# Kernel tuning notes

Measured on AMD Instinct MI355X. Metric: run time of the kernel, lower is better.

The kernel has to match this reference:

```python
import jax, jax.numpy as jnp
import numpy as np

TEMPERATURE = 0.07
NEG = -1e30  # safe stand-in for -inf (keeps grads NaN-free)


def setup_inputs() -> dict:
    key = jax.random.key(0)
    k1, k2 = jax.random.split(key)
    semantic_state = jax.random.normal(k1, (8, 1024, 64), dtype=jnp.float32)
    token_ids = jax.random.randint(k2, (8, 1024), 0, 1000)
    return {"semantic_state": semantic_state, "token_ids": token_ids}


def reference(semantic_state, token_ids):
    # semantic_state: [B, T, D], token_ids: [B, T]
    B, T, D = semantic_state.shape
    N = B * T
    x = semantic_state.reshape(N, D)
    tok = token_ids.reshape(N)

    # L2 normalize (F.normalize, eps=1e-12)
    nrm = jnp.sqrt(jnp.sum(x * x, axis=1, keepdims=True))
    z = x / jnp.maximum(nrm, 1e-12)

    # full cosine-similarity matrix [N, N]
    S = z @ z.T

    # pairs: same token id, excluding self (the per-group similarity structure)
    same = tok[:, None] == tok[None, :]
    eye = jnp.eye(N, dtype=bool)
    mask = same & ~eye

    # per-anchor contrastive term: -logsumexp_{j != i, tok_j == tok_i}(-S_ij / T)
    logits = jnp.where(mask, -S / TEMPERATURE, NEG)
    lse = jax.nn.logsumexp(logits, axis=1)

    valid = mask.any(axis=1)  # anchors whose token repeats (count >= 2)
    per_anchor = jnp.where(valid, -lse, 0.0)

    num_pairs = jnp.sum(mask)  # == sum over groups of N_g*(N_g-1)
    loss = jnp.where(
        num_pairs > 0,
        jnp.sum(per_anchor) / jnp.maximum(num_pairs, 1).astype(S.dtype),
        jnp.array(0.0, dtype=S.dtype),
    )
    return loss
```

## Files before the change

### kernel.cpp

```cpp
#include <hip/hip_runtime.h>
#include <math.h>

#define TEMP 0.07f
#define NTOK 1024
#define CAP 64

__global__ __launch_bounds__(256) void prep_kernel(const float* __restrict__ x,
        const int* __restrict__ tok, float* __restrict__ invn,
        int* __restrict__ cursor, int* __restrict__ bucket, int n) {
    const int lane = threadIdx.x & 63;
    const int w = blockIdx.x * 4 + (threadIdx.x >> 6);
    const int sub = lane & 15, grp = lane >> 4;
    const int row = w * 4 + grp;
    if (row >= n) return;
    float4 v = *(const float4*)&x[row * 64 + sub * 4];
    float s = v.x * v.x + v.y * v.y + v.z * v.z + v.w * v.w;
    s += __shfl_xor(s, 1, 64);
    s += __shfl_xor(s, 2, 64);
    s += __shfl_xor(s, 4, 64);
    s += __shfl_xor(s, 8, 64);
    if (sub == 0) {
        invn[row] = 1.0f / fmaxf(sqrtf(s), 1e-12f);
        int g = tok[row];
        int slot = atomicAdd(&cursor[g], 1);
        if (slot < CAP) bucket[g * CAP + slot] = row;
    }
}

__global__ __launch_bounds__(256) void lse_kernel(const float* __restrict__ x,
        const int* __restrict__ tok, const float* __restrict__ invn,
        const int* __restrict__ cursor, const int* __restrict__ bucket,
        float* __restrict__ per_anchor, int n) {
    const int lane = threadIdx.x & 63;
    const int i = blockIdx.x * 4 + (threadIdx.x >> 6);
    if (i >= n) return;
    const int g = tok[i];
    const int cnt = min(cursor[g], CAP);
    if (cnt < 2) {
        if (lane == 0) per_anchor[i] = 0.0f;
        return;
    }
    const int sub = lane & 15, grp = lane >> 4;
    float4 zi = *(const float4*)&x[i * 64 + sub * 4];
    float sc = invn[i] * (1.0f / TEMP);
    zi.x *= sc; zi.y *= sc; zi.z *= sc; zi.w *= sc;
    const int* bk = &bucket[g * CAP];
    float S = 0.0f;
    for (int m0 = 0; m0 < cnt; m0 += 4) {
        int mm = m0 + grp;
        bool act = (mm < cnt);
        int j = act ? bk[mm] : 0;
        act = act && (j != i);
        float4 zj = *(const float4*)&x[j * 64 + sub * 4];
        float iv = invn[j];
        float d = zi.x * zj.x + zi.y * zj.y + zi.z * zj.z + zi.w * zj.w;
        d += __shfl_xor(d, 1, 64);
        d += __shfl_xor(d, 2, 64);
        d += __shfl_xor(d, 4, 64);
        d += __shfl_xor(d, 8, 64);
        float e = act ? __expf(-d * iv) : 0.0f;
        S += (sub == 0) ? e : 0.0f;
    }
    S += __shfl_xor(S, 16, 64);
    S += __shfl_xor(S, 32, 64);
    if (lane == 0) per_anchor[i] = -__logf(S);
}

__global__ __launch_bounds__(1024) void finalize_kernel(
        const float* __restrict__ per_anchor, const int* __restrict__ cursor,
        float* __restrict__ out, int n) {
    __shared__ double    lr[1024];
    __shared__ long long pr[1024];
    int t = threadIdx.x;
    double s = 0.0;
    const float4* pa4 = (const float4*)per_anchor;
    int n4 = n >> 2;
    for (int k = t; k < n4; k += 1024) {
        float4 v = pa4[k];
        s += (double)v.x + (double)v.y + (double)v.z + (double)v.w;
    }
    for (int k = (n4 << 2) + t; k < n; k += 1024) s += (double)per_anchor[k];
    long long c = cursor[t];
    lr[t] = s;
    pr[t] = c * (c - 1);
    __syncthreads();
    for (int off = 512; off; off >>= 1) {
        if (t < off) { lr[t] += lr[t + off]; pr[t] += pr[t + off]; }
        __syncthreads();
    }
    if (t == 0) out[0] = (pr[0] > 0) ? (float)(lr[0] / (double)pr[0]) : 0.0f;
}

extern "C" void kernel_launch(void* const* d_in, const int* in_sizes, int n_in,
                              void* d_out, int out_size, void* d_ws, size_t ws_size,
                              hipStream_t stream) {
    const float* x = (const float*)d_in[0];
    const int* tok = (const int*)d_in[1];
    int n = in_sizes[1];

    char* ws = (char*)d_ws;
    size_t o = 0;
    int* cursor = (int*)(ws + o);         o += NTOK * 4;
    float* invn = (float*)(ws + o);       o += ((size_t)n * 4 + 255) & ~255UL;
    int* bucket = (int*)(ws + o);         o += (size_t)NTOK * CAP * 4;
    float* per_anchor = (float*)(ws + o);

    hipMemsetAsync(cursor, 0, NTOK * 4, stream);
    prep_kernel<<<(n + 15) / 16, 256, 0, stream>>>(x, tok, invn, cursor, bucket, n);
    lse_kernel<<<(n + 3) / 4, 256, 0, stream>>>(x, tok, invn, cursor, bucket,
                                                per_anchor, n);
    finalize_kernel<<<1, 1024, 0, stream>>>(per_anchor, cursor, (float*)d_out, n);
}
```

Baseline: 22.45 us.

## Fuse final reduction into LSE kernel via last-block atomic counter tree

```diff
diff --git a/kernel.cpp b/kernel.cpp
--- a/kernel.cpp
+++ b/kernel.cpp
@@ -4,6 +4,7 @@
 #define TEMP 0.07f
 #define NTOK 1024
 #define CAP 64
+#define SUBT 64
 
 __global__ __launch_bounds__(256) void prep_kernel(const float* __restrict__ x,
         const int* __restrict__ tok, float* __restrict__ invn,
@@ -27,68 +28,97 @@
     }
 }
 
-__global__ __launch_bounds__(256) void lse_kernel(const float* __restrict__ x,
+__global__ __launch_bounds__(256) void lse_fin_kernel(const float* __restrict__ x,
         const int* __restrict__ tok, const float* __restrict__ invn,
         const int* __restrict__ cursor, const int* __restrict__ bucket,
-        float* __restrict__ per_anchor, int n) {
+        unsigned long long* __restrict__ blk_loss, int* __restrict__ blk_m,
+        unsigned* __restrict__ subt, unsigned* __restrict__ root,
+        float* __restrict__ out, int n) {
     const int lane = threadIdx.x & 63;
-    const int i = blockIdx.x * 4 + (threadIdx.x >> 6);
-    if (i >= n) return;
-    const int g = tok[i];
-    const int cnt = min(cursor[g], CAP);
-    if (cnt < 2) {
-        if (lane == 0) per_anchor[i] = 0.0f;
-        return;
+    const int wid  = threadIdx.x >> 6;
+    const int i = blockIdx.x * 4 + wid;
+    const int nblk = gridDim.x;
+
+    double pa = 0.0;
+    int m = 0;
+    if (i < n) {
+        int g = tok[i];
+        int cnt = min(cursor[g], CAP);
+        if (cnt >= 2) {
+            const int sub = lane & 15, grp = lane >> 4;
+            float4 zi = *(const float4*)&x[i * 64 + sub * 4];
+            float sc = invn[i] * (1.0f / TEMP);
+            zi.x *= sc; zi.y *= sc; zi.z *= sc; zi.w *= sc;
+            const int* bk = &bucket[g * CAP];
+            float S = 0.0f;
+            for (int m0 = 0; m0 < cnt; m0 += 4) {
+                int mm = m0 + grp;
+                bool act = (mm < cnt);
+                int j = act ? bk[mm] : 0;
+                act = act && (j != i);
+                float4 zj = *(const float4*)&x[j * 64 + sub * 4];
+                float iv = invn[j];
+                float d = zi.x * zj.x + zi.y * zj.y + zi.z * zj.z + zi.w * zj.w;
+                d += __shfl_xor(d, 1, 64);
+                d += __shfl_xor(d, 2, 64);
+                d += __shfl_xor(d, 4, 64);
+                d += __shfl_xor(d, 8, 64);
+                float e = act ? __expf(-d * iv) : 0.0f;
+                S += (sub == 0) ? e : 0.0f;
+            }
+            S += __shfl_xor(S, 16, 64);
+            S += __shfl_xor(S, 32, 64);
+            pa = (double)(-__logf(S));
+            m = cnt - 1;
+        }
     }
-    const int sub = lane & 15, grp = lane >> 4;
-    float4 zi = *(const float4*)&x[i * 64 + sub * 4];
-    float sc = invn[i] * (1.0f / TEMP);
-    zi.x *= sc; zi.y *= sc; zi.z *= sc; zi.w *= sc;
-    const int* bk = &bucket[g * CAP];
-    float S = 0.0f;
-    for (int m0 = 0; m0 < cnt; m0 += 4) {
-        int mm = m0 + grp;
-        bool act = (mm < cnt);
-        int j = act ? bk[mm] : 0;
-        act = act && (j != i);
-        float4 zj = *(const float4*)&x[j * 64 + sub * 4];
-        float iv = invn[j];
-        float d = zi.x * zj.x + zi.y * zj.y + zi.z * zj.z + zi.w * zj.w;
-        d += __shfl_xor(d, 1, 64);
-        d += __shfl_xor(d, 2, 64);
-        d += __shfl_xor(d, 4, 64);
-        d += __shfl_xor(d, 8, 64);
-        float e = act ? __expf(-d * iv) : 0.0f;
-        S += (sub == 0) ? e : 0.0f;
+
+    __shared__ double lred[4];
+    __shared__ int    mred[4];
+    __shared__ bool   lastFlag;
+    if (lane == 0) { lred[wid] = pa; mred[wid] = m; }
+    __syncthreads();
+    if (threadIdx.x == 0) {
+        double ls = lred[0] + lred[1] + lred[2] + lred[3];
+        int    ms = mred[0] + mred[1] + mred[2] + mred[3];
+        atomicExch(&blk_loss[blockIdx.x], (unsigned long long)__double_as_longlong(ls));
+        atomicExch(&blk_m[blockIdx.x], ms);
+        __threadfence();
+        int sg = blockIdx.x & (SUBT - 1);
+        int rem = nblk & (SUBT - 1);
+        int quota = nblk / SUBT + (sg < rem ? 1 : 0);
+        bool last = false;
+        unsigned v = atomicAdd(&subt[sg], 1u);
+        if ((int)v == quota - 1) {
+            int nsub = (nblk < SUBT) ? nblk : SUBT;
+            unsigned r = atomicAdd(root, 1u);
+            last = ((int)r == nsub - 1);
+        }
+        lastFlag = last;
     }
-    S += __shfl_xor(S, 16, 64);
-    S += __shfl_xor(S, 32, 64);
-    if (lane == 0) per_anchor[i] = -__logf(S);
-}
+    __syncthreads();
+    if (!lastFlag) return;
 
-__global__ __launch_bounds__(1024) void finalize_kernel(
-        const float* __restrict__ per_anchor, const int* __restrict__ cursor,
-        float* __restrict__ out, int n) {
-    __shared__ double    lr[1024];
-    __shared__ long long pr[1024];
-    int t = threadIdx.x;
-    double s = 0.0;
-    const float4* pa4 = (const float4*)per_anchor;
-    int n4 = n >> 2;
-    for (int k = t; k < n4; k += 1024) {
-        float4 v = pa4[k];
-        s += (double)v.x + (double)v.y + (double)v.z + (double)v.w;
+    double ls = 0.0;
+    long long ps = 0;
+    for (int k = threadIdx.x; k < nblk; k += 256) {
+        ls += __longlong_as_double((long long)atomicAdd(&blk_loss[k], 0ull));
+        ps += (long long)atomicAdd(&blk_m[k], 0);
     }
-    for (int k = (n4 << 2) + t; k < n; k += 1024) s += (double)per_anchor[k];
-    long long c = cursor[t];
-    lr[t] = s;
-    pr[t] = c * (c - 1);
+    __shared__ double    fl[256];
+    __shared__ long long fp[256];
+    fl[threadIdx.x] = ls;
+    fp[threadIdx.x] = ps;
     __syncthreads();
-    for (int off = 512; off; off >>= 1) {
-        if (t < off) { lr[t] += lr[t + off]; pr[t] += pr[t + off]; }
+    for (int off = 128; off; off >>= 1) {
+        if (threadIdx.x < off) {
+            fl[threadIdx.x] += fl[threadIdx.x + off];
+            fp[threadIdx.x] += fp[threadIdx.x + off];
+        }
         __syncthreads();
     }
-    if (t == 0) out[0] = (pr[0] > 0) ? (float)(lr[0] / (double)pr[0]) : 0.0f;
+    if (threadIdx.x == 0)
+        out[0] = (fp[0] > 0) ? (float)(fl[0] / (double)fp[0]) : 0.0f;
 }
 
 extern "C" void kernel_launch(void* const* d_in, const int* in_sizes, int n_in,
@@ -97,17 +127,22 @@
     const float* x = (const float*)d_in[0];
     const int* tok = (const int*)d_in[1];
     int n = in_sizes[1];
+    int nblk = (n + 3) / 4;
 
     char* ws = (char*)d_ws;
     size_t o = 0;
-    int* cursor = (int*)(ws + o);         o += NTOK * 4;
-    float* invn = (float*)(ws + o);       o += ((size_t)n * 4 + 255) & ~255UL;
-    int* bucket = (int*)(ws + o);         o += (size_t)NTOK * CAP * 4;
-    float* per_anchor = (float*)(ws + o);
+    int* cursor = (int*)(ws + o);           o += NTOK * 4;
+    unsigned* subt = (unsigned*)(ws + o);   o += SUBT * 4;
+    unsigned* root = (unsigned*)(ws + o);   o += 256;
+    size_t zero_len = o;
+    float* invn = (float*)(ws + o);         o += ((size_t)n * 4 + 255) & ~255UL;
+    int* bucket = (int*)(ws + o);           o += (size_t)NTOK * CAP * 4;
+    unsigned long long* blk_loss = (unsigned long long*)(ws + o); o += (size_t)nblk * 8;
+    int* blk_m = (int*)(ws + o);
 
-    hipMemsetAsync(cursor, 0, NTOK * 4, stream);
+    hipMemsetAsync(ws, 0, zero_len, stream);
     prep_kernel<<<(n + 15) / 16, 256, 0, stream>>>(x, tok, invn, cursor, bucket, n);
-    lse_kernel<<<(n + 3) / 4, 256, 0, stream>>>(x, tok, invn, cursor, bucket,
-                                                per_anchor, n);
-    finalize_kernel<<<1, 1024, 0, stream>>>(per_anchor, cursor, (float*)d_out, n);
+    lse_fin_kernel<<<nblk, 256, 0, stream>>>(x, tok, invn, cursor, bucket,
+                                             blk_loss, blk_m, subt, root,
+                                             (float*)d_out, n);
 }
```

Result: slower. 53.05 us (+136.3%).

## Use 8 lanes per row with two float4 loads and warp-shuffle final reduction

Applied to the files above, without the earlier changes.

```diff
diff --git a/kernel.cpp b/kernel.cpp
--- a/kernel.cpp
+++ b/kernel.cpp
@@ -10,15 +10,16 @@
         int* __restrict__ cursor, int* __restrict__ bucket, int n) {
     const int lane = threadIdx.x & 63;
     const int w = blockIdx.x * 4 + (threadIdx.x >> 6);
-    const int sub = lane & 15, grp = lane >> 4;
-    const int row = w * 4 + grp;
+    const int sub = lane & 7, mem = lane >> 3;
+    const int row = w * 8 + mem;
     if (row >= n) return;
-    float4 v = *(const float4*)&x[row * 64 + sub * 4];
-    float s = v.x * v.x + v.y * v.y + v.z * v.z + v.w * v.w;
+    const float4* xr = (const float4*)&x[row * 64 + sub * 8];
+    float4 a = xr[0], b = xr[1];
+    float s = a.x * a.x + a.y * a.y + a.z * a.z + a.w * a.w
+            + b.x * b.x + b.y * b.y + b.z * b.z + b.w * b.w;
     s += __shfl_xor(s, 1, 64);
     s += __shfl_xor(s, 2, 64);
     s += __shfl_xor(s, 4, 64);
-    s += __shfl_xor(s, 8, 64);
     if (sub == 0) {
         invn[row] = 1.0f / fmaxf(sqrtf(s), 1e-12f);
         int g = tok[row];
@@ -40,27 +41,31 @@
         if (lane == 0) per_anchor[i] = 0.0f;
         return;
     }
-    const int sub = lane & 15, grp = lane >> 4;
-    float4 zi = *(const float4*)&x[i * 64 + sub * 4];
+    const int sub = lane & 7, mem = lane >> 3;
+    const float4* zr = (const float4*)&x[i * 64 + sub * 8];
+    float4 za = zr[0], zb = zr[1];
     float sc = invn[i] * (1.0f / TEMP);
-    zi.x *= sc; zi.y *= sc; zi.z *= sc; zi.w *= sc;
+    za.x *= sc; za.y *= sc; za.z *= sc; za.w *= sc;
+    zb.x *= sc; zb.y *= sc; zb.z *= sc; zb.w *= sc;
     const int* bk = &bucket[g * CAP];
     float S = 0.0f;
-    for (int m0 = 0; m0 < cnt; m0 += 4) {
-        int mm = m0 + grp;
+    for (int m0 = 0; m0 < cnt; m0 += 8) {
+        int mm = m0 + mem;
         bool act = (mm < cnt);
         int j = act ? bk[mm] : 0;
         act = act && (j != i);
-        float4 zj = *(const float4*)&x[j * 64 + sub * 4];
+        const float4* xr = (const float4*)&x[j * 64 + sub * 8];
+        float4 a = xr[0], b = xr[1];
         float iv = invn[j];
-        float d = zi.x * zj.x + zi.y * zj.y + zi.z * zj.z + zi.w * zj.w;
+        float d = za.x * a.x + za.y * a.y + za.z * a.z + za.w * a.w
+                + zb.x * b.x + zb.y * b.y + zb.z * b.z + zb.w * b.w;
         d += __shfl_xor(d, 1, 64);
         d += __shfl_xor(d, 2, 64);
         d += __shfl_xor(d, 4, 64);
-        d += __shfl_xor(d, 8, 64);
         float e = act ? __expf(-d * iv) : 0.0f;
         S += (sub == 0) ? e : 0.0f;
     }
+    S += __shfl_xor(S, 8, 64);
     S += __shfl_xor(S, 16, 64);
     S += __shfl_xor(S, 32, 64);
     if (lane == 0) per_anchor[i] = -__logf(S);
@@ -69,8 +74,6 @@
 __global__ __launch_bounds__(1024) void finalize_kernel(
         const float* __restrict__ per_anchor, const int* __restrict__ cursor,
         float* __restrict__ out, int n) {
-    __shared__ double    lr[1024];
-    __shared__ long long pr[1024];
     int t = threadIdx.x;
     double s = 0.0;
     const float4* pa4 = (const float4*)per_anchor;
@@ -81,14 +84,27 @@
     }
     for (int k = (n4 << 2) + t; k < n; k += 1024) s += (double)per_anchor[k];
     long long c = cursor[t];
-    lr[t] = s;
-    pr[t] = c * (c - 1);
+    long long p = c * (c - 1);
+    #pragma unroll
+    for (int o = 32; o; o >>= 1) {
+        s += __shfl_xor(s, o, 64);
+        p += __shfl_xor(p, o, 64);
+    }
+    __shared__ double    ls[16];
+    __shared__ long long lp[16];
+    int wid = t >> 6, lane = t & 63;
+    if (lane == 0) { ls[wid] = s; lp[wid] = p; }
     __syncthreads();
-    for (int off = 512; off; off >>= 1) {
-        if (t < off) { lr[t] += lr[t + off]; pr[t] += pr[t + off]; }
-        __syncthreads();
+    if (wid == 0) {
+        double fs = (lane < 16) ? ls[lane] : 0.0;
+        long long fp = (lane < 16) ? lp[lane] : 0;
+        #pragma unroll
+        for (int o = 8; o; o >>= 1) {
+            fs += __shfl_xor(fs, o, 64);
+            fp += __shfl_xor(fp, o, 64);
+        }
+        if (lane == 0) out[0] = (fp > 0) ? (float)(fs / (double)fp) : 0.0f;
     }
-    if (t == 0) out[0] = (pr[0] > 0) ? (float)(lr[0] / (double)pr[0]) : 0.0f;
 }
 
 extern "C" void kernel_launch(void* const* d_in, const int* in_sizes, int n_in,
@@ -106,8 +122,8 @@
     float* per_anchor = (float*)(ws + o);
 
     hipMemsetAsync(cursor, 0, NTOK * 4, stream);
-    prep_kernel<<<(n + 15) / 16, 256, 0, stream>>>(x, tok, invn, cursor, bucket, n);
+    prep_kernel<<<(n + 31) / 32, 256, 0, stream>>>(x, tok, invn, cursor, bucket, n);
     lse_kernel<<<(n + 3) / 4, 256, 0, stream>>>(x, tok, invn, cursor, bucket,
                                                 per_anchor, n);
-    finalize_kernel<<<1, 1024, 0, stream>>>(per_anchor, cursor, (float*)d_out, n);
+    finalize_kernel<<<1, NTOK, 0, stream>>>(per_anchor, cursor, (float*)d_out, n);
 }
```

Result: faster. 21.71 us (-3.3%).
